# Kernel tuning notes

Hardware: AMD Instinct MI355X
Metric: run time of the kernel (lower is better)

The kernel has to match this reference:

```python
import jax, jax.numpy as jnp
import numpy as np

N = 4096  # number of rows == cols (init arg N)
D = 64    # point feature dimension


def setup_inputs() -> dict:
    key = jax.random.key(0)
    kx, ky = jax.random.split(key)
    return {
        "xINP": jax.random.normal(kx, (N, D), dtype=jnp.float32),
        "yINP": jax.random.normal(ky, (N, D), dtype=jnp.float32),
    }


def _pairwise_euclidean(x, y):
    # scipy.spatial.distance_matrix default p=2: sqrt(sum((xi - yj)^2))
    sq = (jnp.sum(x * x, axis=1)[:, None]
          + jnp.sum(y * y, axis=1)[None, :]
          - 2.0 * (x @ y.T))
    return jnp.sqrt(jnp.maximum(sq, 0.0))  # [N, N]


def _greedy_match(cost):
    # Greedy bipartite matching: visit all (i, j) pairs in ascending cost
    # order; accept a pair iff both row i and col j are still unmatched.
    n, m = cost.shape
    order = jnp.argsort(cost.reshape(-1))          # stable sort, like python sorted
    rows = (order // m).astype(jnp.int32)          # [n*m]
    cols = (order % m).astype(jnp.int32)           # [n*m]

    def step(carry, ij):
        rm, cm = carry
        i, j = ij
        free = (rm[i] == -1) & (cm[j] == -1)
        rm = rm.at[i].set(jnp.where(free, j, rm[i]))
        cm = cm.at[j].set(jnp.where(free, i, cm[j]))
        return (rm, cm), None

    init = (jnp.full((n,), -1, dtype=jnp.int32),   # row_to_col_match_vec
            jnp.full((m,), -1, dtype=jnp.int32))   # col_to_row_match_vec
    (_, cm), _ = jax.lax.scan(step, init, (rows, cols))
    return cm


def reference(xINP, yINP):
    cost = _pairwise_euclidean(xINP, yINP)   # [N, N]
    return _greedy_match(cost)               # [N] int32: col_to_row_match_vec
```

## Files before the change

kernel.cpp:

```cpp
#include <hip/hip_runtime.h>
#include <stdint.h>

#define NN 4096
#define DD 64
#define GCOL 16
#define CCH 16
#define TMAX 112
#define ROUNDS_FAST 22
#define ROUNDS_FB 32

typedef unsigned long long u64;
typedef unsigned int u32;

#define RESC 0xFFFFFFFFFFFFFFFEull
#define EMPTY (~0ull)

__device__ __forceinline__ u64 pk(float d, u32 idx) {
  return (((u64)__float_as_uint(d)) << 32) | (u64)idx;
}

__device__ __forceinline__ float distfly(const float* __restrict__ x,
                                         const float* __restrict__ y,
                                         float xxi, float yyj, int i, int j) {
  const float* xi = x + (size_t)i * DD;
  const float* yj = y + (size_t)j * DD;
  float dot = 0.f;
#pragma unroll
  for (int k = 0; k < DD; ++k) dot = fmaf(xi[k], yj[k], dot);
  float sq = (xxi + yyj) - 2.0f * dot;
  return sqrtf(fmaxf(sq, 0.f));
}

__global__ void k_init(const float* __restrict__ x, const float* __restrict__ y,
                       float* xx, float* yy, int* rm, int* cm, int* FR, int* Fcnt,
                       u64* rowbest, u64* colpart) {
  int i = blockIdx.x * blockDim.x + threadIdx.x;
  if (i < NN) {
    const float* xi = x + (size_t)i * DD;
    const float* yi = y + (size_t)i * DD;
    float sx = 0.f, sy = 0.f;
#pragma unroll
    for (int k = 0; k < DD; ++k) { sx = fmaf(xi[k], xi[k], sx); sy = fmaf(yi[k], yi[k], sy); }
    xx[i] = sx; yy[i] = sy;
    rm[i] = -1; cm[i] = -1; FR[i] = i;
    rowbest[i] = ~0ull;
#pragma unroll
    for (int g = 0; g < CCH; ++g) colpart[(size_t)g * NN + i] = RESC;
    if (i == 0) *Fcnt = NN;
  }
}

__global__ void k_build(const float* __restrict__ x, const float* __restrict__ y,
                        const float* __restrict__ xx, const float* __restrict__ yy,
                        float* __restrict__ C) {
  __shared__ float xs[64][65];
  __shared__ float ys[64][65];
  int t = threadIdx.x;
  int bi = blockIdx.y * 64, bj = blockIdx.x * 64;
  for (int e = t; e < 64 * 64; e += 256) {
    int r = e >> 6, c = e & 63;
    xs[r][c] = x[(size_t)(bi + r) * DD + c];
    ys[r][c] = y[(size_t)(bj + r) * DD + c];
  }
  __syncthreads();
  int tx = t & 15, ty = t >> 4;
  float acc[4][4];
#pragma unroll
  for (int r = 0; r < 4; ++r)
#pragma unroll
    for (int c = 0; c < 4; ++c) acc[r][c] = 0.f;
#pragma unroll
  for (int k = 0; k < 64; ++k) {
    float a[4], b[4];
#pragma unroll
    for (int r = 0; r < 4; ++r) a[r] = xs[ty * 4 + r][k];
#pragma unroll
    for (int c = 0; c < 4; ++c) b[c] = ys[tx * 4 + c][k];
#pragma unroll
    for (int r = 0; r < 4; ++r)
#pragma unroll
      for (int c = 0; c < 4; ++c) acc[r][c] = fmaf(a[r], b[c], acc[r][c]);
  }
#pragma unroll
  for (int r = 0; r < 4; ++r) {
    int i = bi + ty * 4 + r;
    float xxi = xx[i];
    float4 v;
    float* vp = (float*)&v;
#pragma unroll
    for (int c = 0; c < 4; ++c) {
      int j = bj + tx * 4 + c;
      float sq = (xxi + yy[j]) - 2.0f * acc[r][c];
      vp[c] = sqrtf(fmaxf(sq, 0.f));
    }
    *(float4*)(C + (size_t)i * NN + bj + tx * 4) = v;
  }
}

__global__ void k_round(const float* __restrict__ C, const int* __restrict__ rm,
                        const int* __restrict__ cm, u64* __restrict__ rowbest,
                        u64* __restrict__ colpart) {
  __shared__ u64 red[256];
  __shared__ u64 part[4][64];
  int b = blockIdx.x;
  int t = threadIdx.x;
  if (b < NN) {
    int i = b;
    if (rm[i] != -1) return;
    u64 e = rowbest[i];
    u32 jb = (u32)e;
    if (jb < NN && cm[jb] == -1) return;
    const float* Ci = C + (size_t)i * NN;
    u64 best = ~0ull;
    for (int j0 = t * 4; j0 < NN; j0 += 1024) {
      float4 v = *(const float4*)(Ci + j0);
      int4 m = *(const int4*)(cm + j0);
      const float* vp = (const float*)&v;
      const int* mp = (const int*)&m;
#pragma unroll
      for (int c = 0; c < 4; ++c) {
        if (mp[c] == -1) {
          u64 key = pk(vp[c], (u32)(j0 + c));
          if (key < best) best = key;
        }
      }
    }
    red[t] = best;
    __syncthreads();
    for (int s = 128; s > 0; s >>= 1) {
      if (t < s) { if (red[t + s] < red[t]) red[t] = red[t + s]; }
      __syncthreads();
    }
    if (t == 0) rowbest[i] = red[0];
  } else {
    int idx = b - NN;
    int cb = idx & 63, g = idx >> 6;
    int lane = t & 63, s = t >> 6;
    int j = cb * 64 + lane;
    u64* slot = colpart + (size_t)g * NN + j;
    bool stale = false;
    if (cm[j] == -1) {
      u64 e = *slot;
      if (e != EMPTY) {
        u32 io = (u32)e;
        stale = !(io < NN && rm[io] == -1);
      }
    }
    u64 best = ~0ull;
    if (stale) {
      int i0 = g * 256 + s * 64;
      for (int i = i0; i < i0 + 64; ++i) {
        if (rm[i] != -1) continue;
        u64 key = pk(C[(size_t)i * NN + j], (u32)i);
        if (key < best) best = key;
      }
    }
    part[s][lane] = best;
    __syncthreads();
    if (s == 0 && stale) {
      u64 b0 = part[0][lane];
#pragma unroll
      for (int q = 1; q < 4; ++q) if (part[q][lane] < b0) b0 = part[q][lane];
      *slot = b0;
    }
  }
}

__global__ void k_accept3(const u64* __restrict__ colpart, const u64* __restrict__ rowbest,
                          int* rm, int* cm, int* Fcnt) {
  if (*Fcnt == 0) return;
  int j = blockIdx.x * 256 + threadIdx.x;
  if (cm[j] != -1) return;
  u64 best = ~0ull;
#pragma unroll
  for (int g = 0; g < CCH; ++g) {
    u64 v = colpart[(size_t)g * NN + j];
    if (v < best) best = v;
  }
  if (best == ~0ull) return;
  int i = (int)(u32)best;
  if ((u32)(rowbest[i] & 0xffffffffu) == (u32)j) {
    rm[i] = j; cm[j] = i;
    atomicSub(Fcnt, 1);
  }
}

__global__ __launch_bounds__(256) void k_endgame(const float* __restrict__ C,
                                                 int* rm, int* cm, int* FRg) {
  __shared__ float Csub[TMAX * TMAX];
  __shared__ int sF, sG, sc_star, scnt;
  __shared__ int sFR[TMAX], sFC[TMAX];
  __shared__ u64 rkey[TMAX];
  __shared__ int rcol[TMAX];
  __shared__ int cfree[TMAX];
  __shared__ u64 wred[4];
  __shared__ u64 red[256];
  int t = threadIdx.x;
  if (t == 0) { sF = 0; sG = 0; }
  __syncthreads();
  for (int i = t; i < NN; i += 256)
    if (rm[i] == -1) { int p = atomicAdd(&sF, 1); if (p < TMAX) sFR[p] = i; }
  for (int j = t; j < NN; j += 256)
    if (cm[j] == -1) { int p = atomicAdd(&sG, 1); if (p < TMAX) sFC[p] = j; }
  __syncthreads();
  int F = sF;
  if (F == 0) return;
  if (F <= TMAX) {
    for (int r = (t >> 6); r < F; r += 4) {
      const float* Ci = C + (size_t)sFR[r] * NN;
      for (int c = (t & 63); c < F; c += 64) Csub[r * F + c] = Ci[sFC[c]];
    }
    for (int c = t; c < F; c += 256) cfree[c] = 1;
    __syncthreads();
    for (int r = t; r < F; r += 256) {
      const float* row = Csub + r * F;
      u64 bk = ~0ull; int bc = 0; int ig = sFR[r];
      for (int c = 0; c < F; ++c) {
        u64 k = (((u64)__float_as_uint(row[c])) << 24) | (u32)(ig * NN + sFC[c]);
        if (k < bk) { bk = k; bc = c; }
      }
      rkey[r] = bk; rcol[r] = bc;
    }
    __syncthreads();
    for (int it = 0; it < F; ++it) {
      u64 kb = ~0ull;
      if (t < F && rkey[t] != ~0ull) kb = (rkey[t] << 8) | (u64)(u32)t;
      for (int s = 32; s > 0; s >>= 1) {
        u64 o = __shfl_down(kb, s, 64);
        if (o < kb) kb = o;
      }
      if ((t & 63) == 0) wred[t >> 6] = kb;
      __syncthreads();
      if (t == 0) {
        u64 b = wred[0];
#pragma unroll
        for (int wv = 1; wv < 4; ++wv) if (wred[wv] < b) b = wred[wv];
        int rstar = (int)(b & 255);
        if (rstar >= F) rstar = 0;
        int cstar = rcol[rstar];
        sc_star = cstar;
        int i = sFR[rstar], j = sFC[cstar];
        rm[i] = j; cm[j] = i;
        rkey[rstar] = ~0ull; cfree[cstar] = 0;
      }
      __syncthreads();
      int cs = sc_star;
      for (int r = t; r < F; r += 256) {
        if (rkey[r] != ~0ull && rcol[r] == cs) {
          const float* row = Csub + r * F;
          u64 bk = ~0ull; int bc = 0; int ig = sFR[r];
          for (int c = 0; c < F; ++c) {
            if (!cfree[c]) continue;
            u64 k = (((u64)__float_as_uint(row[c])) << 24) | (u32)(ig * NN + sFC[c]);
            if (k < bk) { bk = k; bc = c; }
          }
          rkey[r] = bk; rcol[r] = bc;
        }
      }
      __syncthreads();
    }
  } else {
    for (int it = 0; it < NN; ++it) {
      if (t == 0) scnt = 0;
      __syncthreads();
      for (int i = t; i < NN; i += 256)
        if (rm[i] == -1) { int p = atomicAdd(&scnt, 1); FRg[p] = i; }
      __syncthreads();
      int Fa = scnt;
      if (Fa == 0) break;
      u64 best = ~0ull;
      int total = Fa * NN;
      for (int idx = t; idx < total; idx += 256) {
        int b = idx >> 12, j = idx & 4095;
        if (cm[j] != -1) continue;
        int i = FRg[b];
        u64 key = pk(C[(size_t)i * NN + j], (u32)(i * NN + j));
        if (key < best) best = key;
      }
      red[t] = best;
      __syncthreads();
      for (int s = 128; s > 0; s >>= 1) {
        if (t < s) { if (red[t + s] < red[t]) red[t] = red[t + s]; }
        __syncthreads();
      }
      if (t == 0) {
        u32 lo = (u32)red[0];
        rm[lo >> 12] = lo & 4095; cm[lo & 4095] = lo >> 12;
      }
      __syncthreads();
    }
  }
}

template <bool USEC>
__global__ void k_rowpass(const float* __restrict__ C,
                          const float* __restrict__ x, const float* __restrict__ y,
                          const float* __restrict__ xx, const float* __restrict__ yy,
                          const int* __restrict__ cm, const int* __restrict__ FR,
                          const int* __restrict__ Fcnt, u64* __restrict__ rowbest) {
  int b = blockIdx.x;
  if (b >= *Fcnt) return;
  int i = FR[b];
  __shared__ float xsh[DD];
  __shared__ u64 red[256];
  int t = threadIdx.x;
  if (!USEC) { if (t < DD) xsh[t] = x[(size_t)i * DD + t]; }
  __syncthreads();
  float xxi = xx[i];
  u64 best = ~0ull;
  for (int j = t; j < NN; j += 256) {
    if (cm[j] != -1) continue;
    float d;
    if (USEC) {
      d = C[(size_t)i * NN + j];
    } else {
      const float* yj = y + (size_t)j * DD;
      float dot = 0.f;
#pragma unroll
      for (int k = 0; k < DD; ++k) dot = fmaf(xsh[k], yj[k], dot);
      float sq = (xxi + yy[j]) - 2.0f * dot;
      d = sqrtf(fmaxf(sq, 0.f));
    }
    u64 key = pk(d, (u32)j);
    if (key < best) best = key;
  }
  red[t] = best;
  __syncthreads();
  for (int s = 128; s > 0; s >>= 1) {
    if (t < s) { if (red[t + s] < red[t]) red[t] = red[t + s]; }
    __syncthreads();
  }
  if (t == 0) rowbest[i] = red[0];
}

template <bool USEC>
__global__ void k_colpass(const float* __restrict__ C,
                          const float* __restrict__ x, const float* __restrict__ y,
                          const float* __restrict__ xx, const float* __restrict__ yy,
                          const int* __restrict__ cm, const int* __restrict__ FR,
                          const int* __restrict__ Fcnt, u64* __restrict__ colpart) {
  int t = threadIdx.x;
  int j = blockIdx.x * 256 + t;
  int g = blockIdx.y;
  int F = *Fcnt;
  if (F == 0) return;
  int b0 = (g * F) / GCOL, b1 = ((g + 1) * F) / GCOL;
  u64 best = ~0ull;
  if (cm[j] == -1) {
    float yyj = yy[j];
    if (USEC) {
      for (int b = b0; b < b1; ++b) {
        int i = FR[b];
        u64 key = pk(C[(size_t)i * NN + j], (u32)i);
        if (key < best) best = key;
      }
    } else {
      float4 yr[16];
      const float4* yj4 = (const float4*)(y + (size_t)j * DD);
#pragma unroll
      for (int q = 0; q < 16; ++q) yr[q] = yj4[q];
      for (int b = b0; b < b1; ++b) {
        int i = FR[b];
        const float4* xi4 = (const float4*)(x + (size_t)i * DD);
        float dot = 0.f;
#pragma unroll
        for (int q = 0; q < 16; ++q) {
          float4 a = xi4[q], bb = yr[q];
          dot = fmaf(a.x, bb.x, dot); dot = fmaf(a.y, bb.y, dot);
          dot = fmaf(a.z, bb.z, dot); dot = fmaf(a.w, bb.w, dot);
        }
        float sq = (xx[i] + yyj) - 2.0f * dot;
        float d = sqrtf(fmaxf(sq, 0.f));
        u64 key = pk(d, (u32)i);
        if (key < best) best = key;
      }
    }
  }
  colpart[(size_t)g * NN + j] = best;
}

__global__ void k_accept(const u64* __restrict__ colpart, const u64* __restrict__ rowbest,
                         int* rm, int* cm, int* FR, int* Fcnt) {
  __shared__ int scnt;
  int t = threadIdx.x;
  if (*Fcnt == 0) return;
  for (int j = t; j < NN; j += 1024) {
    if (cm[j] != -1) continue;
    u64 best = ~0ull;
#pragma unroll
    for (int g = 0; g < GCOL; ++g) {
      u64 v = colpart[(size_t)g * NN + j];
      if (v < best) best = v;
    }
    if (best == ~0ull) continue;
    int i = (int)(u32)best;
    if ((u32)(rowbest[i] & 0xffffffffu) == (u32)j) { rm[i] = j; cm[j] = i; }
  }
  __syncthreads();
  if (t == 0) scnt = 0;
  __syncthreads();
  for (int i = t; i < NN; i += 1024)
    if (rm[i] == -1) { int p = atomicAdd(&scnt, 1); FR[p] = i; }
  __syncthreads();
  if (t == 0) *Fcnt = scnt;
}

template <bool USEC>
__global__ void k_cleanup(const float* __restrict__ C,
                          const float* __restrict__ x, const float* __restrict__ y,
                          const float* __restrict__ xx, const float* __restrict__ yy,
                          int* rm, int* cm, int* FR) {
  __shared__ int scnt;
  __shared__ u64 red[1024];
  int t = threadIdx.x;
  for (int it = 0; it < NN; ++it) {
    if (t == 0) scnt = 0;
    __syncthreads();
    for (int i = t; i < NN; i += 1024)
      if (rm[i] == -1) { int p = atomicAdd(&scnt, 1); FR[p] = i; }
    __syncthreads();
    int F = scnt;
    if (F == 0) break;
    u64 best = ~0ull;
    int total = F * NN;
    for (int idx = t; idx < total; idx += 1024) {
      int b = idx >> 12;
      int j = idx & 4095;
      if (cm[j] != -1) continue;
      int i = FR[b];
      float d;
      if (USEC) d = C[(size_t)i * NN + j];
      else d = distfly(x, y, xx[i], yy[j], i, j);
      u64 key = pk(d, (u32)(i * NN + j));
      if (key < best) best = key;
    }
    red[t] = best;
    __syncthreads();
    for (int s = 512; s > 0; s >>= 1) {
      if (t < s) { if (red[t + s] < red[t]) red[t] = red[t + s]; }
      __syncthreads();
    }
    if (t == 0) {
      u32 lo = (u32)red[0];
      int i = lo >> 12, j = lo & 4095;
      rm[i] = j; cm[j] = i;
    }
    __syncthreads();
  }
}

extern "C" void kernel_launch(void* const* d_in, const int* in_sizes, int n_in,
                              void* d_out, int out_size, void* d_ws, size_t ws_size,
                              hipStream_t stream) {
  const float* x = (const float*)d_in[0];
  const float* y = (const float*)d_in[1];
  int* cm = (int*)d_out;

  char* w = (char*)d_ws;
  float* xx = (float*)(w + 0);
  float* yy = (float*)(w + 16384);
  int* rm = (int*)(w + 32768);
  int* FR = (int*)(w + 49152);
  int* Fcnt = (int*)(w + 65536);
  u64* rowbest = (u64*)(w + 65664);
  u64* colpart = (u64*)(w + 98432);
  float* C = (float*)(w + 1048576);

  size_t need = 1048576 + (size_t)NN * NN * 4;
  bool usec = ws_size >= need;

  k_init<<<dim3(16), 256, 0, stream>>>(x, y, xx, yy, rm, cm, FR, Fcnt, rowbest, colpart);
  if (usec) {
    k_build<<<dim3(64, 64), 256, 0, stream>>>(x, y, xx, yy, C);
    for (int r = 0; r < ROUNDS_FAST; ++r) {
      k_round<<<dim3(NN + 64 * CCH), 256, 0, stream>>>(C, rm, cm, rowbest, colpart);
      k_accept3<<<dim3(16), 256, 0, stream>>>(colpart, rowbest, rm, cm, Fcnt);
    }
    k_endgame<<<dim3(1), 256, 0, stream>>>(C, rm, cm, FR);
  } else {
    for (int r = 0; r < ROUNDS_FB; ++r) {
      k_rowpass<false><<<dim3(NN), 256, 0, stream>>>(nullptr, x, y, xx, yy, cm, FR, Fcnt, rowbest);
      k_colpass<false><<<dim3(16, GCOL), 256, 0, stream>>>(nullptr, x, y, xx, yy, cm, FR, Fcnt, colpart);
      k_accept<<<dim3(1), 1024, 0, stream>>>(colpart, rowbest, rm, cm, FR, Fcnt);
    }
    k_cleanup<false><<<dim3(1), 1024, 0, stream>>>(nullptr, x, y, xx, yy, rm, cm, FR);
  }
}
```

Measured before the change: 672.3 us.

## Fuse initial row/column minima into build and rescan only stale row chunks

```diff
diff --git a/kernel.cpp b/kernel.cpp
--- a/kernel.cpp
+++ b/kernel.cpp
@@ -5,8 +5,9 @@
 #define DD 64
 #define GCOL 16
 #define CCH 16
+#define RCHK 8
 #define TMAX 112
-#define ROUNDS_FAST 22
+#define ROUNDS_FAST 17
 #define ROUNDS_FB 32
 
 typedef unsigned long long u64;
@@ -33,7 +34,7 @@
 
 __global__ void k_init(const float* __restrict__ x, const float* __restrict__ y,
                        float* xx, float* yy, int* rm, int* cm, int* FR, int* Fcnt,
-                       u64* rowbest, u64* colpart) {
+                       u64* rowbest, u64* rowpart, u64* colpart) {
   int i = blockIdx.x * blockDim.x + threadIdx.x;
   if (i < NN) {
     const float* xi = x + (size_t)i * DD;
@@ -45,16 +46,20 @@
     rm[i] = -1; cm[i] = -1; FR[i] = i;
     rowbest[i] = ~0ull;
 #pragma unroll
-    for (int g = 0; g < CCH; ++g) colpart[(size_t)g * NN + i] = RESC;
+    for (int h = 0; h < RCHK; ++h) rowpart[(size_t)h * NN + i] = ~0ull;
+#pragma unroll
+    for (int g = 0; g < CCH; ++g) colpart[(size_t)g * NN + i] = ~0ull;
     if (i == 0) *Fcnt = NN;
   }
 }
 
 __global__ void k_build(const float* __restrict__ x, const float* __restrict__ y,
                         const float* __restrict__ xx, const float* __restrict__ yy,
-                        float* __restrict__ C) {
+                        float* __restrict__ C, u64* __restrict__ rowbest,
+                        u64* __restrict__ rowpart, u64* __restrict__ colpart) {
   __shared__ float xs[64][65];
   __shared__ float ys[64][65];
+  __shared__ u64 colred[16][65];
   int t = threadIdx.x;
   int bi = blockIdx.y * 64, bj = blockIdx.x * 64;
   for (int e = t; e < 64 * 64; e += 256) {
@@ -81,73 +86,111 @@
 #pragma unroll
       for (int c = 0; c < 4; ++c) acc[r][c] = fmaf(a[r], b[c], acc[r][c]);
   }
+  u64 ck[4] = {~0ull, ~0ull, ~0ull, ~0ull};
+  int hrow = bj >> 9;
+  int gcol = bi >> 8;
 #pragma unroll
   for (int r = 0; r < 4; ++r) {
     int i = bi + ty * 4 + r;
     float xxi = xx[i];
     float4 v;
     float* vp = (float*)&v;
+    u64 rkey = ~0ull;
 #pragma unroll
     for (int c = 0; c < 4; ++c) {
       int j = bj + tx * 4 + c;
       float sq = (xxi + yy[j]) - 2.0f * acc[r][c];
-      vp[c] = sqrtf(fmaxf(sq, 0.f));
+      float d = sqrtf(fmaxf(sq, 0.f));
+      vp[c] = d;
+      u64 kr = pk(d, (u32)j);
+      if (kr < rkey) rkey = kr;
+      u64 kc = pk(d, (u32)i);
+      if (kc < ck[c]) ck[c] = kc;
     }
     *(float4*)(C + (size_t)i * NN + bj + tx * 4) = v;
-  }
-}
-
-__global__ void k_round(const float* __restrict__ C, const int* __restrict__ rm,
-                        const int* __restrict__ cm, u64* __restrict__ rowbest,
-                        u64* __restrict__ colpart) {
+#pragma unroll
+    for (int md = 1; md < 16; md <<= 1) {
+      u64 o = __shfl_xor(rkey, md, 64);
+      if (o < rkey) rkey = o;
+    }
+    if (tx == 0) {
+      atomicMin(&rowpart[(size_t)hrow * NN + i], rkey);
+      atomicMin(&rowbest[i], rkey);
+    }
+  }
+#pragma unroll
+  for (int c = 0; c < 4; ++c) colred[ty][tx * 4 + c] = ck[c];
+  __syncthreads();
+  if (t < 64) {
+    u64 m = colred[0][t];
+#pragma unroll
+    for (int k = 1; k < 16; ++k) if (colred[k][t] < m) m = colred[k][t];
+    atomicMin(&colpart[(size_t)gcol * NN + bj + t], m);
+  }
+}
+
+__global__ void k_round2(const float* __restrict__ C, const int* __restrict__ rm,
+                         const int* __restrict__ cm, u64* __restrict__ rowbest,
+                         u64* __restrict__ rowpart, u64* __restrict__ colpart) {
   __shared__ u64 red[256];
+  __shared__ u64 rp[RCHK];
+  __shared__ int stale[RCHK];
   __shared__ u64 part[4][64];
   int b = blockIdx.x;
   int t = threadIdx.x;
   if (b < NN) {
     int i = b;
     if (rm[i] != -1) return;
-    u64 e = rowbest[i];
-    u32 jb = (u32)e;
+    u64 rb = rowbest[i];
+    u32 jb = (u32)rb;
     if (jb < NN && cm[jb] == -1) return;
+    if (t < RCHK) {
+      u64 e = rowpart[(size_t)t * NN + i];
+      rp[t] = e;
+      u32 je = (u32)e;
+      stale[t] = (e != EMPTY) && !(je < NN && cm[je] == -1);
+    }
+    __syncthreads();
     const float* Ci = C + (size_t)i * NN;
-    u64 best = ~0ull;
-    for (int j0 = t * 4; j0 < NN; j0 += 1024) {
-      float4 v = *(const float4*)(Ci + j0);
-      int4 m = *(const int4*)(cm + j0);
-      const float* vp = (const float*)&v;
-      const int* mp = (const int*)&m;
-#pragma unroll
-      for (int c = 0; c < 4; ++c) {
-        if (mp[c] == -1) {
-          u64 key = pk(vp[c], (u32)(j0 + c));
-          if (key < best) best = key;
-        }
-      }
-    }
-    red[t] = best;
-    __syncthreads();
-    for (int s = 128; s > 0; s >>= 1) {
-      if (t < s) { if (red[t + s] < red[t]) red[t] = red[t + s]; }
-      __syncthreads();
-    }
-    if (t == 0) rowbest[i] = red[0];
+    for (int h = 0; h < RCHK; ++h) {
+      if (!stale[h]) continue;
+      int j0 = h * 512 + t * 2;
+      float2 v = *(const float2*)(Ci + j0);
+      int2 m = *(const int2*)(cm + j0);
+      u64 best = ~0ull;
+      if (m.x == -1) best = pk(v.x, (u32)j0);
+      if (m.y == -1) { u64 k2 = pk(v.y, (u32)(j0 + 1)); if (k2 < best) best = k2; }
+      red[t] = best;
+      __syncthreads();
+      for (int s = 128; s > 0; s >>= 1) {
+        if (t < s) { if (red[t + s] < red[t]) red[t] = red[t + s]; }
+        __syncthreads();
+      }
+      if (t == 0) { rp[h] = red[0]; rowpart[(size_t)h * NN + i] = red[0]; }
+      __syncthreads();
+    }
+    if (t == 0) {
+      u64 best = rp[0];
+#pragma unroll
+      for (int h = 1; h < RCHK; ++h) if (rp[h] < best) best = rp[h];
+      rowbest[i] = best;
+    }
   } else {
     int idx = b - NN;
     int cb = idx & 63, g = idx >> 6;
     int lane = t & 63, s = t >> 6;
     int j = cb * 64 + lane;
     u64* slot = colpart + (size_t)g * NN + j;
-    bool stale = false;
+    bool stale_c = false;
     if (cm[j] == -1) {
       u64 e = *slot;
       if (e != EMPTY) {
         u32 io = (u32)e;
-        stale = !(io < NN && rm[io] == -1);
+        stale_c = !(io < NN && rm[io] == -1);
       }
     }
     u64 best = ~0ull;
-    if (stale) {
+    if (stale_c) {
       int i0 = g * 256 + s * 64;
       for (int i = i0; i < i0 + 64; ++i) {
         if (rm[i] != -1) continue;
@@ -157,7 +200,7 @@
     }
     part[s][lane] = best;
     __syncthreads();
-    if (s == 0 && stale) {
+    if (s == 0 && stale_c) {
       u64 b0 = part[0][lane];
 #pragma unroll
       for (int q = 1; q < 4; ++q) if (part[q][lane] < b0) b0 = part[q][lane];
@@ -463,17 +506,20 @@
   int* FR = (int*)(w + 49152);
   int* Fcnt = (int*)(w + 65536);
   u64* rowbest = (u64*)(w + 65664);
-  u64* colpart = (u64*)(w + 98432);
+  u64* rowpart = (u64*)(w + 98432);
+  u64* colpart = (u64*)(w + 360704);
   float* C = (float*)(w + 1048576);
 
   size_t need = 1048576 + (size_t)NN * NN * 4;
   bool usec = ws_size >= need;
 
-  k_init<<<dim3(16), 256, 0, stream>>>(x, y, xx, yy, rm, cm, FR, Fcnt, rowbest, colpart);
+  k_init<<<dim3(16), 256, 0, stream>>>(x, y, xx, yy, rm, cm, FR, Fcnt,
+                                       rowbest, rowpart, colpart);
   if (usec) {
-    k_build<<<dim3(64, 64), 256, 0, stream>>>(x, y, xx, yy, C);
+    k_build<<<dim3(64, 64), 256, 0, stream>>>(x, y, xx, yy, C, rowbest, rowpart, colpart);
+    k_accept3<<<dim3(16), 256, 0, stream>>>(colpart, rowbest, rm, cm, Fcnt);
     for (int r = 0; r < ROUNDS_FAST; ++r) {
-      k_round<<<dim3(NN + 64 * CCH), 256, 0, stream>>>(C, rm, cm, rowbest, colpart);
+      k_round2<<<dim3(NN + 64 * CCH), 256, 0, stream>>>(C, rm, cm, rowbest, rowpart, colpart);
       k_accept3<<<dim3(16), 256, 0, stream>>>(colpart, rowbest, rm, cm, Fcnt);
     }
     k_endgame<<<dim3(1), 256, 0, stream>>>(C, rm, cm, FR);
```

New measurement: 1.510 ms. +124.6%, slower.
